# Kernel tuning notes

Hardware: AMD Instinct MI355X
Metric: run time of the kernel (lower is better)

## Reference

```python
import jax, jax.numpy as jnp
import numpy as np
import math

B, T, E, H = 8, 1024, 768, 12
D = E // H  # 64

def setup_inputs() -> dict:
    key = jax.random.key(0)
    ks = jax.random.split(key, 5)
    return {
        "x": jax.random.normal(ks[0], (B, T, E), dtype=jnp.float32),
        "w_attn": jax.random.normal(ks[1], (E, 3 * E), dtype=jnp.float32) * 0.02,
        "b_attn": jax.random.normal(ks[2], (3 * E,), dtype=jnp.float32) * 0.02,
        "w_proj": jax.random.normal(ks[3], (E, E), dtype=jnp.float32) * 0.02,
        "b_proj": jax.random.normal(ks[4], (E,), dtype=jnp.float32) * 0.02,
    }

def reference(x, w_attn, b_attn, w_proj, b_proj):
    b, t, e = x.shape
    h, d = H, E // H
    qkv = x @ w_attn + b_attn                      # [B,T,3E]
    q, k, v = jnp.split(qkv, 3, axis=2)
    q = q.reshape(b, t, h, d).transpose(0, 2, 1, 3)  # [B,H,T,D]
    k = k.reshape(b, t, h, d).transpose(0, 2, 1, 3)
    v = v.reshape(b, t, h, d).transpose(0, 2, 1, 3)
    scores = jnp.einsum('bhqd,bhkd->bhqk', q, k)     # [B,H,T,T]
    causal = jnp.tril(jnp.ones((t, t), dtype=bool))
    scores = jnp.where(causal[None, None], scores, -jnp.inf)
    attn = jax.nn.softmax(scores / jnp.float32(math.sqrt(d)), axis=-1)
    out = jnp.einsum('bhqk,bhkd->bhqd', attn, v)     # [B,H,T,D]
    out = out.transpose(0, 2, 1, 3).reshape(b, t, h * d)
    return out @ w_proj + b_proj
```

## Files before the change

### kernel.cpp

```cpp
#include <hip/hip_runtime.h>
#include <math.h>


#define B_ 8
#define T_ 1024
#define E_ 768
#define H_ 12
#define D_ 64
#define E3 (3 * E_)

typedef __attribute__((ext_vector_type(8))) short bf16x8;
typedef __attribute__((ext_vector_type(4))) float f32x4;

#define SCALE 0.18033688f

__device__ __forceinline__ unsigned short f2bf(float f) {
    unsigned int u = __builtin_bit_cast(unsigned int, f);
    u += 0x7fffu + ((u >> 16) & 1u);
    return (unsigned short)(u >> 16);
}

__device__ __forceinline__ void async_copy16(void* lds, const void* g) {
    __builtin_amdgcn_global_load_lds(
        (const __attribute__((address_space(1))) void*)g,
        (__attribute__((address_space(3))) void*)lds, 16, 0, 0);
}

#define NCVT 6144
#define NTA  (72 * 24)
#define NTP  (24 * 24)

__device__ __forceinline__ void transpose_tile(
    const float* __restrict__ W, unsigned short* __restrict__ Wt,
    int K, int N, int gx, int gy, unsigned short (*tile)[33])
{
    const int n0 = gx * 32, k0 = gy * 32;
    const int tx = threadIdx.x & 31, ty = threadIdx.x >> 5;
    #pragma unroll
    for (int i = 0; i < 4; ++i)
        tile[ty + i * 8][tx] = f2bf(W[(size_t)(k0 + ty + i * 8) * N + n0 + tx]);
    __syncthreads();
    #pragma unroll
    for (int i = 0; i < 4; ++i)
        Wt[(size_t)(n0 + ty + i * 8) * K + k0 + tx] = tile[tx][ty + i * 8];
}

__global__ __launch_bounds__(256) void prep_kernel(
    const float* __restrict__ x, unsigned short* __restrict__ x_bf,
    const float* __restrict__ w_attn, unsigned short* __restrict__ wat,
    const float* __restrict__ w_proj, unsigned short* __restrict__ wpt)
{
    __shared__ unsigned short tile[32][33];
    const int bid = blockIdx.x;
    if (bid < NCVT) {
        const int i = bid * 256 + threadIdx.x;
        float4 f = ((const float4*)x)[i];
        ushort4 o;
        o.x = f2bf(f.x); o.y = f2bf(f.y); o.z = f2bf(f.z); o.w = f2bf(f.w);
        ((ushort4*)x_bf)[i] = o;
    } else if (bid < NCVT + NTA) {
        const int t = bid - NCVT;
        transpose_tile(w_attn, wat, E_, E3, t % 72, t / 72, tile);
    } else {
        const int t = bid - NCVT - NTA;
        transpose_tile(w_proj, wpt, E_, E_, t % 24, t / 24, tile);
    }
}


__global__ __launch_bounds__(512, 4) void gemm_qkv_128x192(
    const unsigned short* __restrict__ A,
    const unsigned short* __restrict__ Wt,
    const float* __restrict__ bias,
    unsigned short* __restrict__ C,
    unsigned short* __restrict__ vt)
{
    constexpr int K = 768;
    constexpr int N = E3;
    constexpr int NKT = 12;

    extern __shared__ unsigned short lds[];

    const int tid  = threadIdx.x;
    const int lane = tid & 63;
    const int w    = tid >> 6;
    const int wm   = w >> 2;
    const int wn   = w & 3;
    const int n16  = lane & 15;
    const int quad = lane >> 4;
    const int l7   = lane & 7;
    const int lrow = lane >> 3;
    const int lcol = (l7 ^ lrow) * 8;

    const int lin  = blockIdx.x;
    const int s    = lin >> 3;
    const int by   = (lin & 7) * 8 + s / 12;
    const int bx   = s % 12;
    const int bm = by * 128, bn = bx * 192;

    const unsigned short* Asrc = A  + (size_t)(bm + lrow) * K + lcol;
    const unsigned short* Bsrc = Wt + (size_t)(bn + lrow) * K + lcol;

    auto stage = [&](int bi, int kt) {
        unsigned short* ab = lds + (bi ? 8192 : 0);
        unsigned short* bb = lds + 16384 + (bi ? 12288 : 0);
        #pragma unroll
        for (int i = 0; i < 2; ++i) {
            const int c = w * 2 + i;
            async_copy16(&ab[c * 512], Asrc + (size_t)(c * 8) * K + kt * 64);
        }
        #pragma unroll
        for (int i = 0; i < 3; ++i) {
            const int c = w * 3 + i;
            async_copy16(&bb[c * 512], Bsrc + (size_t)(c * 8) * K + kt * 64);
        }
    };

    f32x4 acc[4][3] = {};

#define BARR  __builtin_amdgcn_s_barrier()
#define VM5   asm volatile("s_waitcnt vmcnt(5)" ::: "memory")
#define VM0   asm volatile("s_waitcnt vmcnt(0)" ::: "memory")
#define PRI1  __builtin_amdgcn_s_setprio(1)
#define PRI0  __builtin_amdgcn_s_setprio(0)

    stage(0, 0);

    #pragma unroll 1
    for (int u = 0; u < NKT; ++u) {
        const int bi = u & 1;
        const unsigned short* ab = lds + (bi ? 8192 : 0);
        const unsigned short* bb = lds + 16384 + (bi ? 12288 : 0);
        if (u < NKT - 1) {
            stage(bi ^ 1, u + 1);
            VM5;
        } else {
            VM0;
        }
        BARR;

        #pragma unroll
        for (int kc = 0; kc < 2; ++kc) {
            bf16x8 af[4], bf[3];
            #pragma unroll
            for (int m = 0; m < 4; ++m) {
                const int r = wm * 16 + m * 32 + n16;
                af[m] = *(const bf16x8*)&ab[r * 64 + (((kc * 4 + quad) ^ (r & 7)) * 8)];
            }
            #pragma unroll
            for (int n = 0; n < 3; ++n) {
                const int r = wn * 16 + n * 64 + n16;
                bf[n] = *(const bf16x8*)&bb[r * 64 + (((kc * 4 + quad) ^ (r & 7)) * 8)];
            }
            PRI1;
            #pragma unroll
            for (int m = 0; m < 4; ++m)
                #pragma unroll
                for (int n = 0; n < 3; ++n)
                    acc[m][n] = __builtin_amdgcn_mfma_f32_16x16x32_bf16(
                        af[m], bf[n], acc[m][n], 0, 0, 0);
            PRI0;
        }
        BARR;
    }

#undef VM5
#undef VM0

    if (bx >= 8) {
        #pragma unroll
        for (int m = 0; m < 4; ++m) {
            const int tt = bm + wm * 16 + m * 32 + quad * 4;
            const size_t bb2 = (size_t)(tt >> 10) * 768;
            const int tin = tt & 1023;
            #pragma unroll
            for (int n = 0; n < 3; ++n) {
                const int col = bn + wn * 16 + n * 64 + n16;
                const int ch = col - 1536;
                const float bv = bias[col];
                ushort4 o4;
                o4.x = f2bf(acc[m][n][0] + bv);
                o4.y = f2bf(acc[m][n][1] + bv);
                o4.z = f2bf(acc[m][n][2] + bv);
                o4.w = f2bf(acc[m][n][3] + bv);
                *(ushort4*)&vt[(bb2 + ch) * 1024 + tin] = o4;
            }
        }
    } else {
        const bool scale_q = bx < 4;
        #pragma unroll
        for (int m = 0; m < 4; ++m) {
            #pragma unroll
            for (int r = 0; r < 4; ++r) {
                const size_t rowoff = (size_t)(bm + wm * 16 + m * 32 + quad * 4 + r) * N;
                #pragma unroll
                for (int n = 0; n < 3; ++n) {
                    const int col = bn + wn * 16 + n * 64 + n16;
                    float v = acc[m][n][r] + bias[col];
                    if (scale_q) v *= SCALE;
                    C[rowoff + col] = f2bf(v);
                }
            }
        }
    }
}

template <typename OutT, int MODE, int BM, int BN, int WR, int WC>
__global__ __launch_bounds__(256) void gemm_mfma_kernel(
    const unsigned short* __restrict__ A,
    const unsigned short* __restrict__ Wt,
    const float* __restrict__ bias,
    OutT* __restrict__ C,
    unsigned short* __restrict__ vt,
    int M, int N, int K)
{
    constexpr int MT = BM / WR / 16;
    constexpr int NT = BN / WC / 16;
    constexpr int CA = BM / 32;
    constexpr int CB = BN / 32;
    constexpr int QBX = 768 / BN;
    constexpr int VBX = 1536 / BN;

    __shared__ unsigned short Abuf[BM * 64];
    __shared__ unsigned short Bbuf[BN * 64];

    const int tid = threadIdx.x;
    const int lane = tid & 63;
    const int w = tid >> 6;
    const int n16 = lane & 15;
    const int quad = lane >> 4;

    const int nbx = gridDim.x;
    const int lin = blockIdx.y * nbx + blockIdx.x;
    const int band_sz = 8 * nbx;
    const int band = lin / band_sz;
    const int rr = lin % band_sz;
    const int bm = (band * 8 + (rr & 7)) * BM;
    const int bx = rr >> 3;
    const int bn = bx * BN;

    const int wmbase = (w / WC) * (BM / WR);
    const int wnbase = (w % WC) * (BN / WC);

    const int lrow = lane >> 3;
    const int lcol = ((lane & 7) ^ lrow) * 8;

    f32x4 acc[MT][NT] = {};

    for (int k0 = 0; k0 < K; k0 += 64) {
        __syncthreads();
        #pragma unroll
        for (int i = 0; i < CA; ++i) {
            const int c = w * CA + i;
            const int row = c * 8 + lrow;
            async_copy16(&Abuf[c * 512], A + (size_t)(bm + row) * K + k0 + lcol);
        }
        #pragma unroll
        for (int i = 0; i < CB; ++i) {
            const int c = w * CB + i;
            const int row = c * 8 + lrow;
            async_copy16(&Bbuf[c * 512], Wt + (size_t)(bn + row) * K + k0 + lcol);
        }
        __syncthreads();

        #pragma unroll
        for (int kc = 0; kc < 2; ++kc) {
            bf16x8 af[MT], bf[NT];
            #pragma unroll
            for (int mt = 0; mt < MT; ++mt) {
                const int r = wmbase + mt * 16 + n16;
                af[mt] = *(const bf16x8*)&Abuf[r * 64 + ((kc * 4 + quad) ^ (r & 7)) * 8];
            }
            #pragma unroll
            for (int nt = 0; nt < NT; ++nt) {
                const int r = wnbase + nt * 16 + n16;
                bf[nt] = *(const bf16x8*)&Bbuf[r * 64 + ((kc * 4 + quad) ^ (r & 7)) * 8];
            }
            #pragma unroll
            for (int mt = 0; mt < MT; ++mt)
                #pragma unroll
                for (int nt = 0; nt < NT; ++nt)
                    acc[mt][nt] = __builtin_amdgcn_mfma_f32_16x16x32_bf16(
                        af[mt], bf[nt], acc[mt][nt], 0, 0, 0);
        }
    }

    if (MODE == 1 && bx >= VBX) {
        #pragma unroll
        for (int mt = 0; mt < MT; ++mt) {
            const int tt = bm + wmbase + mt * 16 + quad * 4;
            const size_t bb = (size_t)(tt >> 10) * 768;
            const int tin = tt & 1023;
            #pragma unroll
            for (int nt = 0; nt < NT; ++nt) {
                const int col = bn + wnbase + nt * 16 + n16;
                const int ch = col - 1536;
                const float bv = bias[col];
                ushort4 o4;
                o4.x = f2bf(acc[mt][nt][0] + bv);
                o4.y = f2bf(acc[mt][nt][1] + bv);
                o4.z = f2bf(acc[mt][nt][2] + bv);
                o4.w = f2bf(acc[mt][nt][3] + bv);
                *(ushort4*)&vt[(bb + ch) * 1024 + tin] = o4;
            }
        }
        return;
    }

    const bool scale_q = (MODE == 1) && (bx < QBX);
    #pragma unroll
    for (int mt = 0; mt < MT; ++mt) {
        #pragma unroll
        for (int r = 0; r < 4; ++r) {
            const size_t rowoff = (size_t)(bm + wmbase + mt * 16 + quad * 4 + r) * N;
            #pragma unroll
            for (int nt = 0; nt < NT; ++nt) {
                const int col = bn + wnbase + nt * 16 + n16;
                float v = acc[mt][nt][r] + bias[col];
                if (scale_q) v *= SCALE;
                if constexpr (sizeof(OutT) == 2) C[rowoff + col] = (OutT)f2bf(v);
                else                             C[rowoff + col] = (OutT)v;
            }
        }
    }
}

#define BKEY 128

__global__ __launch_bounds__(256, 3) void flash_attn_kernel(
    const unsigned short* __restrict__ qkv,
    const unsigned short* __restrict__ vt,
    unsigned short* __restrict__ out)
{
    __shared__ __align__(16) unsigned short Ks[2][BKEY * 64];
    __shared__ __align__(16) unsigned short Vts[64 * BKEY];

    const int tid = threadIdx.x;
    const int idx = blockIdx.x;
    const int xcd = idx & 7;
    const int j   = idx >> 3;
    const int head = xcd * 12 + (j % 12);
    const int p    = j / 12;
    const int h = head % H_;
    const int b = head / H_;

    const int lane = tid & 63;
    const int w    = tid >> 6;
    const int n16  = lane & 15;
    const int quad = lane >> 4;

    const size_t base = (size_t)b * T_ * E3;
    const unsigned short* qbase = qkv + base + h * D_;
    const unsigned short* kbase = qkv + base + E_ + h * D_;
    const unsigned short* vtb   = vt + (size_t)(b * H_ + h) * 64 * 1024;

    const int lrow = lane >> 3;
    const int lcol = ((lane & 7) ^ lrow) * 8;
    const int vr4 = lane >> 4;
    const int vc  = lane & 15;

    const int qtA = p, qtB = 15 - p;
    const int nIterA = (qtA + 2) >> 1;
    const int nIterB = (qtB + 2) >> 1;
    const int wqA = qtA * 64 + w * 16;
    const int wqB = qtB * 64 + w * 16;

    const unsigned short* qrpA = qbase + (size_t)(wqA + n16) * E3 + quad * 8;
    bf16x8 qfA0 = *(const bf16x8*)qrpA;
    bf16x8 qfA1 = *(const bf16x8*)(qrpA + 32);
    const unsigned short* qrpB = qbase + (size_t)(wqB + n16) * E3 + quad * 8;
    bf16x8 qfB0 = *(const bf16x8*)qrpB;
    bf16x8 qfB1 = *(const bf16x8*)(qrpB + 32);

    f32x4 oA[4] = {}, oB[4] = {};
    float lsA = 0.f, lsB = 0.f;

    const int sLo = n16 + 32 * (quad & 1);
    const int sHi = sLo + 16;
    const bool hiSel = quad >= 2;

    auto stageK = [&](int t) {
        unsigned short* dst = Ks[t & 1];
        const int k0 = t * BKEY;
        #pragma unroll
        for (int i = 0; i < 4; ++i) {
            const int c = w * 4 + i;
            const int row = c * 8 + lrow;
            async_copy16(&dst[c * 512], kbase + (size_t)(k0 + row) * E3 + lcol);
        }
    };
    auto stageV = [&](int t) {
        const int k0 = t * BKEY;
        #pragma unroll
        for (int i = 0; i < 4; ++i) {
            const int jj = w * 4 + i;
            const int row = 4 * jj + vr4;
            async_copy16(&Vts[4 * jj * BKEY],
                         vtb + (size_t)row * 1024 + k0 + ((vc ^ (row & 15)) * 8));
        }
    };

    auto phase = [&](bf16x8 qf0, bf16x8 qf1, f32x4* o, float& lsum,
                     int wave_q_min, int k0, const unsigned short* Kb,
                     bool doMid, bool notLast) {
        int knt_lim = ((wave_q_min + 15 - k0) >> 4) + 1;
        if (knt_lim > 8) knt_lim = 8;
        const int ks_lim = (knt_lim + 1) >> 1;
        const int nkp = ks_lim * 2;
        int Ab2 = wave_q_min - k0 - 15;
        int kfull = Ab2 < 0 ? 0 : (Ab2 >> 4) + 1;
        if (kfull > 8) kfull = 8;

        const int qcol = wave_q_min + n16;

        f32x4 s[8];
        #pragma unroll
        for (int knt = 0; knt < 8; ++knt) {
            if (knt < knt_lim) {
                const int r = knt * 16 + n16;
                bf16x8 kf0 = *(const bf16x8*)&Kb[r * 64 + ((0 + quad) ^ (r & 7)) * 8];
                bf16x8 kf1 = *(const bf16x8*)&Kb[r * 64 + ((4 + quad) ^ (r & 7)) * 8];
                f32x4 acc = {0.f, 0.f, 0.f, 0.f};
                acc = __builtin_amdgcn_mfma_f32_16x16x32_bf16(kf0, qf0, acc, 0, 0, 0);
                acc = __builtin_amdgcn_mfma_f32_16x16x32_bf16(kf1, qf1, acc, 0, 0, 0);
                s[knt] = acc;
            }
        }
        #pragma unroll
        for (int knt = 0; knt < 8; ++knt) {
            if (knt >= kfull && knt < nkp) {
                const int krow = k0 + knt * 16 + quad * 4;
                #pragma unroll
                for (int r = 0; r < 4; ++r) {
                    float v = (knt < knt_lim) ? s[knt][r] : -1e30f;
                    if (krow + r > qcol) v = -1e30f;
                    s[knt][r] = v;
                }
            }
        }

        unsigned int e0[8], e1[8];
        #pragma unroll
        for (int knt = 0; knt < 8; ++knt) {
            if (knt < nkp) {
                float pv0 = __builtin_amdgcn_exp2f(s[knt][0]);
                float pv1 = __builtin_amdgcn_exp2f(s[knt][1]);
                float pv2 = __builtin_amdgcn_exp2f(s[knt][2]);
                float pv3 = __builtin_amdgcn_exp2f(s[knt][3]);
                lsum += (pv0 + pv1) + (pv2 + pv3);
                unsigned int u0 = __builtin_bit_cast(unsigned int, pv0);
                unsigned int u1 = __builtin_bit_cast(unsigned int, pv1);
                unsigned int u2 = __builtin_bit_cast(unsigned int, pv2);
                unsigned int u3 = __builtin_bit_cast(unsigned int, pv3);
                e0[knt] = ((u0 + 0x8000u) >> 16) | ((u1 + 0x8000u) & 0xffff0000u);
                e1[knt] = ((u2 + 0x8000u) >> 16) | ((u3 + 0x8000u) & 0xffff0000u);
            }
        }

        if (doMid) {
            if (notLast) asm volatile("s_waitcnt vmcnt(4)" ::: "memory");
            else         asm volatile("s_waitcnt vmcnt(0)" ::: "memory");
            __builtin_amdgcn_s_barrier();
        }

        #pragma unroll
        for (int ks = 0; ks < 4; ++ks) {
            if (ks < ks_lim) {
                const int kA = 2 * ks, kB = 2 * ks + 1;
                unsigned int a0 = (unsigned)__shfl((int)e0[kA], sLo);
                unsigned int a1 = (unsigned)__shfl((int)e1[kA], sLo);
                unsigned int a2 = (unsigned)__shfl((int)e0[kA], sHi);
                unsigned int a3 = (unsigned)__shfl((int)e1[kA], sHi);
                unsigned int b0 = (unsigned)__shfl((int)e0[kB], sLo);
                unsigned int b1 = (unsigned)__shfl((int)e1[kB], sLo);
                unsigned int b2 = (unsigned)__shfl((int)e0[kB], sHi);
                unsigned int b3 = (unsigned)__shfl((int)e1[kB], sHi);
                uint4 pu;
                pu.x = hiSel ? b0 : a0;
                pu.y = hiSel ? b1 : a1;
                pu.z = hiSel ? b2 : a2;
                pu.w = hiSel ? b3 : a3;
                bf16x8 pf = __builtin_bit_cast(bf16x8, pu);
                #pragma unroll
                for (int dt = 0; dt < 4; ++dt) {
                    const int row = dt * 16 + n16;
                    bf16x8 vf = *(const bf16x8*)&Vts[row * BKEY +
                                    (((ks * 4 + quad) ^ n16) * 8)];
                    o[dt] = __builtin_amdgcn_mfma_f32_16x16x32_bf16(pf, vf, o[dt], 0, 0, 0);
                }
            }
        }
    };

    stageK(0);
    asm volatile("s_waitcnt vmcnt(0)" ::: "memory");
    __builtin_amdgcn_s_barrier();

    for (int it = 0; it < nIterB; ++it) {
        const int k0 = it * BKEY;
        const bool notLast = (it + 1 < nIterB);

        stageV(it);
        if (notLast) stageK(it + 1);
        const unsigned short* Kb = Ks[it & 1];

        phase(qfB0, qfB1, oB, lsB, wqB, k0, Kb, true,  notLast);
        if (it < nIterA)
            phase(qfA0, qfA1, oA, lsA, wqA, k0, Kb, false, notLast);

        asm volatile("s_waitcnt vmcnt(0)" ::: "memory");
        __builtin_amdgcn_s_barrier();
    }

    lsA += __shfl_xor(lsA, 16); lsA += __shfl_xor(lsA, 32);
    lsB += __shfl_xor(lsB, 16); lsB += __shfl_xor(lsB, 32);

    #pragma unroll
    for (int r = 0; r < 4; ++r) {
        const float invA = 1.f / __shfl(lsA, quad * 4 + r);
        unsigned short* orowA = out + ((size_t)b * T_ + wqA + quad * 4 + r) * E_ + h * D_;
        #pragma unroll
        for (int dt = 0; dt < 4; ++dt)
            orowA[dt * 16 + n16] = f2bf(oA[dt][r] * invA);
        const float invB = 1.f / __shfl(lsB, quad * 4 + r);
        unsigned short* orowB = out + ((size_t)b * T_ + wqB + quad * 4 + r) * E_ + h * D_;
        #pragma unroll
        for (int dt = 0; dt < 4; ++dt)
            orowB[dt * 16 + n16] = f2bf(oB[dt][r] * invB);
    }
}

extern "C" void kernel_launch(void* const* d_in, const int* in_sizes, int n_in,
                              void* d_out, int out_size, void* d_ws, size_t ws_size,
                              hipStream_t stream)
{
    const float* x      = (const float*)d_in[0];
    const float* w_attn = (const float*)d_in[1];
    const float* b_attn = (const float*)d_in[2];
    const float* w_proj = (const float*)d_in[3];
    const float* b_proj = (const float*)d_in[4];
    float* out = (float*)d_out;

    const int M = B_ * T_;

    unsigned short* x_bf   = (unsigned short*)d_ws;
    unsigned short* wat    = x_bf + (size_t)M * E_;
    unsigned short* wpt    = wat + (size_t)E3 * E_;
    unsigned short* qkv_bf = wpt + (size_t)E_ * E_;
    unsigned short* att_bf = qkv_bf + (size_t)M * E3;
    unsigned short* vt_bf  = att_bf + (size_t)M * E_;

    static bool qkv_attr_set = false;
    if (!qkv_attr_set) {
        (void)hipFuncSetAttribute((const void*)gemm_qkv_128x192,
                                  hipFuncAttributeMaxDynamicSharedMemorySize, 81920);
        qkv_attr_set = true;
    }

    prep_kernel<<<NCVT + NTA + NTP, 256, 0, stream>>>(x, x_bf, w_attn, wat, w_proj, wpt);

    gemm_qkv_128x192<<<dim3(768), dim3(512), 81920, stream>>>(
        x_bf, wat, b_attn, qkv_bf, vt_bf);

    flash_attn_kernel<<<B_ * H_ * 8, 256, 0, stream>>>(qkv_bf, vt_bf, att_bf);

    gemm_mfma_kernel<float, 0, 64, 128, 2, 2>
        <<<dim3(E_ / 128, M / 64), 256, 0, stream>>>(
        att_bf, wpt, b_proj, out, nullptr, M, E_, E_);
}
```

Baseline: 167.2 us.

## Unify QKV and output projections into one templated double-buffered 128x96 GEMM

Replaces the 512-thread 128x192 QKV GEMM and the single-buffered 64x128 output-projection GEMM with one templated 256-thread kernel using 128x96 tiles and double-buffered async global-to-LDS loads. The output projection gains load/compute overlap it lacked before, and the QKV GEMM now runs more, smaller blocks. The hipFuncSetAttribute call for 81920 bytes of dynamic LDS is removed because the new kernel requests 57344 bytes. Smaller N tiles lower per-block reuse of the A operand and raise the number of barriers per output element.

```diff
diff --git a/kernel.cpp b/kernel.cpp
--- a/kernel.cpp
+++ b/kernel.cpp
@@ -68,58 +68,64 @@
 }
 
 
-__global__ __launch_bounds__(512, 4) void gemm_qkv_128x192(
+template <typename OutT, int MODE, int N_>
+__global__ __launch_bounds__(256, 2) void gemm_2ph(
     const unsigned short* __restrict__ A,
     const unsigned short* __restrict__ Wt,
     const float* __restrict__ bias,
-    unsigned short* __restrict__ C,
+    OutT* __restrict__ C,
     unsigned short* __restrict__ vt)
 {
     constexpr int K = 768;
-    constexpr int N = E3;
     constexpr int NKT = 12;
+    constexpr int NBX = N_ / 96;
+    constexpr int QBX = 768 / 96;
+    constexpr int VBX = 1536 / 96;
 
     extern __shared__ unsigned short lds[];
 
     const int tid  = threadIdx.x;
     const int lane = tid & 63;
     const int w    = tid >> 6;
-    const int wm   = w >> 2;
-    const int wn   = w & 3;
+    const int wm   = w >> 1;
+    const int wn   = w & 1;
     const int n16  = lane & 15;
     const int quad = lane >> 4;
-    const int l7   = lane & 7;
-    const int lrow = lane >> 3;
-    const int lcol = (l7 ^ lrow) * 8;
-
-    const int lin  = blockIdx.x;
-    const int s    = lin >> 3;
-    const int by   = (lin & 7) * 8 + s / 12;
-    const int bx   = s % 12;
-    const int bm = by * 128, bn = bx * 192;
-
-    const unsigned short* Asrc = A  + (size_t)(bm + lrow) * K + lcol;
-    const unsigned short* Bsrc = Wt + (size_t)(bn + lrow) * K + lcol;
+
+    const int lin = blockIdx.x;
+    const int s   = lin >> 3;
+    const int by  = (lin & 7) * 8 + s / NBX;
+    const int bx  = s % NBX;
+    const int bm = by * 128, bn = bx * 96;
+
+    const unsigned short* Asrc = A  + (size_t)bm * K;
+    const unsigned short* Bsrc = Wt + (size_t)bn * K;
 
     auto stage = [&](int bi, int kt) {
         unsigned short* ab = lds + (bi ? 8192 : 0);
-        unsigned short* bb = lds + 16384 + (bi ? 12288 : 0);
-        #pragma unroll
-        for (int i = 0; i < 2; ++i) {
-            const int c = w * 2 + i;
-            async_copy16(&ab[c * 512], Asrc + (size_t)(c * 8) * K + kt * 64);
+        unsigned short* bb = lds + 16384 + (bi ? 6144 : 0);
+        #pragma unroll
+        for (int i = 0; i < 4; ++i) {
+            const int li = i * 256 + tid;
+            const int row = li >> 3;
+            const int sl  = li & 7;
+            async_copy16(&ab[li * 8],
+                         Asrc + (size_t)row * K + ((sl ^ (row & 7)) * 8) + kt * 64);
         }
         #pragma unroll
         for (int i = 0; i < 3; ++i) {
-            const int c = w * 3 + i;
-            async_copy16(&bb[c * 512], Bsrc + (size_t)(c * 8) * K + kt * 64);
+            const int li = i * 256 + tid;
+            const int row = li >> 3;
+            const int sl  = li & 7;
+            async_copy16(&bb[li * 8],
+                         Bsrc + (size_t)row * K + ((sl ^ (row & 7)) * 8) + kt * 64);
         }
     };
 
     f32x4 acc[4][3] = {};
 
 #define BARR  __builtin_amdgcn_s_barrier()
-#define VM5   asm volatile("s_waitcnt vmcnt(5)" ::: "memory")
+#define VM7   asm volatile("s_waitcnt vmcnt(7)" ::: "memory")
 #define VM0   asm volatile("s_waitcnt vmcnt(0)" ::: "memory")
 #define PRI1  __builtin_amdgcn_s_setprio(1)
 #define PRI0  __builtin_amdgcn_s_setprio(0)
@@ -130,10 +136,10 @@
     for (int u = 0; u < NKT; ++u) {
         const int bi = u & 1;
         const unsigned short* ab = lds + (bi ? 8192 : 0);
-        const unsigned short* bb = lds + 16384 + (bi ? 12288 : 0);
+        const unsigned short* bb = lds + 16384 + (bi ? 6144 : 0);
         if (u < NKT - 1) {
             stage(bi ^ 1, u + 1);
-            VM5;
+            VM7;
         } else {
             VM0;
         }
@@ -149,7 +155,7 @@
             }
             #pragma unroll
             for (int n = 0; n < 3; ++n) {
-                const int r = wn * 16 + n * 64 + n16;
+                const int r = wn * 16 + n * 32 + n16;
                 bf[n] = *(const bf16x8*)&bb[r * 64 + (((kc * 4 + quad) ^ (r & 7)) * 8)];
             }
             PRI1;
@@ -164,10 +170,10 @@
         BARR;
     }
 
-#undef VM5
+#undef VM7
 #undef VM0
 
-    if (bx >= 8) {
+    if (MODE == 1 && bx >= VBX) {
         #pragma unroll
         for (int m = 0; m < 4; ++m) {
             const int tt = bm + wm * 16 + m * 32 + quad * 4;
@@ -175,7 +181,7 @@
             const int tin = tt & 1023;
             #pragma unroll
             for (int n = 0; n < 3; ++n) {
-                const int col = bn + wn * 16 + n * 64 + n16;
+                const int col = bn + wn * 16 + n * 32 + n16;
                 const int ch = col - 1536;
                 const float bv = bias[col];
                 ushort4 o4;
@@ -186,137 +192,19 @@
                 *(ushort4*)&vt[(bb2 + ch) * 1024 + tin] = o4;
             }
         }
-    } else {
-        const bool scale_q = bx < 4;
-        #pragma unroll
-        for (int m = 0; m < 4; ++m) {
-            #pragma unroll
-            for (int r = 0; r < 4; ++r) {
-                const size_t rowoff = (size_t)(bm + wm * 16 + m * 32 + quad * 4 + r) * N;
-                #pragma unroll
-                for (int n = 0; n < 3; ++n) {
-                    const int col = bn + wn * 16 + n * 64 + n16;
-                    float v = acc[m][n][r] + bias[col];
-                    if (scale_q) v *= SCALE;
-                    C[rowoff + col] = f2bf(v);
-                }
-            }
-        }
-    }
-}
-
-template <typename OutT, int MODE, int BM, int BN, int WR, int WC>
-__global__ __launch_bounds__(256) void gemm_mfma_kernel(
-    const unsigned short* __restrict__ A,
-    const unsigned short* __restrict__ Wt,
-    const float* __restrict__ bias,
-    OutT* __restrict__ C,
-    unsigned short* __restrict__ vt,
-    int M, int N, int K)
-{
-    constexpr int MT = BM / WR / 16;
-    constexpr int NT = BN / WC / 16;
-    constexpr int CA = BM / 32;
-    constexpr int CB = BN / 32;
-    constexpr int QBX = 768 / BN;
-    constexpr int VBX = 1536 / BN;
-
-    __shared__ unsigned short Abuf[BM * 64];
-    __shared__ unsigned short Bbuf[BN * 64];
-
-    const int tid = threadIdx.x;
-    const int lane = tid & 63;
-    const int w = tid >> 6;
-    const int n16 = lane & 15;
-    const int quad = lane >> 4;
-
-    const int nbx = gridDim.x;
-    const int lin = blockIdx.y * nbx + blockIdx.x;
-    const int band_sz = 8 * nbx;
-    const int band = lin / band_sz;
-    const int rr = lin % band_sz;
-    const int bm = (band * 8 + (rr & 7)) * BM;
-    const int bx = rr >> 3;
-    const int bn = bx * BN;
-
-    const int wmbase = (w / WC) * (BM / WR);
-    const int wnbase = (w % WC) * (BN / WC);
-
-    const int lrow = lane >> 3;
-    const int lcol = ((lane & 7) ^ lrow) * 8;
-
-    f32x4 acc[MT][NT] = {};
-
-    for (int k0 = 0; k0 < K; k0 += 64) {
-        __syncthreads();
-        #pragma unroll
-        for (int i = 0; i < CA; ++i) {
-            const int c = w * CA + i;
-            const int row = c * 8 + lrow;
-            async_copy16(&Abuf[c * 512], A + (size_t)(bm + row) * K + k0 + lcol);
-        }
-        #pragma unroll
-        for (int i = 0; i < CB; ++i) {
-            const int c = w * CB + i;
-            const int row = c * 8 + lrow;
-            async_copy16(&Bbuf[c * 512], Wt + (size_t)(bn + row) * K + k0 + lcol);
-        }
-        __syncthreads();
-
-        #pragma unroll
-        for (int kc = 0; kc < 2; ++kc) {
-            bf16x8 af[MT], bf[NT];
-            #pragma unroll
-            for (int mt = 0; mt < MT; ++mt) {
-                const int r = wmbase + mt * 16 + n16;
-                af[mt] = *(const bf16x8*)&Abuf[r * 64 + ((kc * 4 + quad) ^ (r & 7)) * 8];
-            }
-            #pragma unroll
-            for (int nt = 0; nt < NT; ++nt) {
-                const int r = wnbase + nt * 16 + n16;
-                bf[nt] = *(const bf16x8*)&Bbuf[r * 64 + ((kc * 4 + quad) ^ (r & 7)) * 8];
-            }
-            #pragma unroll
-            for (int mt = 0; mt < MT; ++mt)
-                #pragma unroll
-                for (int nt = 0; nt < NT; ++nt)
-                    acc[mt][nt] = __builtin_amdgcn_mfma_f32_16x16x32_bf16(
-                        af[mt], bf[nt], acc[mt][nt], 0, 0, 0);
-        }
-    }
-
-    if (MODE == 1 && bx >= VBX) {
-        #pragma unroll
-        for (int mt = 0; mt < MT; ++mt) {
-            const int tt = bm + wmbase + mt * 16 + quad * 4;
-            const size_t bb = (size_t)(tt >> 10) * 768;
-            const int tin = tt & 1023;
-            #pragma unroll
-            for (int nt = 0; nt < NT; ++nt) {
-                const int col = bn + wnbase + nt * 16 + n16;
-                const int ch = col - 1536;
-                const float bv = bias[col];
-                ushort4 o4;
-                o4.x = f2bf(acc[mt][nt][0] + bv);
-                o4.y = f2bf(acc[mt][nt][1] + bv);
-                o4.z = f2bf(acc[mt][nt][2] + bv);
-                o4.w = f2bf(acc[mt][nt][3] + bv);
-                *(ushort4*)&vt[(bb + ch) * 1024 + tin] = o4;
-            }
-        }
         return;
     }
 
     const bool scale_q = (MODE == 1) && (bx < QBX);
     #pragma unroll
-    for (int mt = 0; mt < MT; ++mt) {
+    for (int m = 0; m < 4; ++m) {
         #pragma unroll
         for (int r = 0; r < 4; ++r) {
-            const size_t rowoff = (size_t)(bm + wmbase + mt * 16 + quad * 4 + r) * N;
+            const size_t rowoff = (size_t)(bm + wm * 16 + m * 32 + quad * 4 + r) * N_;
             #pragma unroll
-            for (int nt = 0; nt < NT; ++nt) {
-                const int col = bn + wnbase + nt * 16 + n16;
-                float v = acc[mt][nt][r] + bias[col];
+            for (int n = 0; n < 3; ++n) {
+                const int col = bn + wn * 16 + n * 32 + n16;
+                float v = acc[m][n][r] + bias[col];
                 if (scale_q) v *= SCALE;
                 if constexpr (sizeof(OutT) == 2) C[rowoff + col] = (OutT)f2bf(v);
                 else                             C[rowoff + col] = (OutT)v;
@@ -550,21 +438,13 @@
     unsigned short* att_bf = qkv_bf + (size_t)M * E3;
     unsigned short* vt_bf  = att_bf + (size_t)M * E_;
 
-    static bool qkv_attr_set = false;
-    if (!qkv_attr_set) {
-        (void)hipFuncSetAttribute((const void*)gemm_qkv_128x192,
-                                  hipFuncAttributeMaxDynamicSharedMemorySize, 81920);
-        qkv_attr_set = true;
-    }
-
     prep_kernel<<<NCVT + NTA + NTP, 256, 0, stream>>>(x, x_bf, w_attn, wat, w_proj, wpt);
 
-    gemm_qkv_128x192<<<dim3(768), dim3(512), 81920, stream>>>(
+    gemm_2ph<unsigned short, 1, E3><<<dim3(1536), dim3(256), 57344, stream>>>(
         x_bf, wat, b_attn, qkv_bf, vt_bf);
 
     flash_attn_kernel<<<B_ * H_ * 8, 256, 0, stream>>>(qkv_bf, vt_bf, att_bf);
 
-    gemm_mfma_kernel<float, 0, 64, 128, 2, 2>
-        <<<dim3(E_ / 128, M / 64), 256, 0, stream>>>(
-        att_bf, wpt, b_proj, out, nullptr, M, E_, E_);
-}
+    gemm_2ph<float, 0, E_><<<dim3(512), dim3(256), 57344, stream>>>(
+        att_bf, wpt, b_proj, out, nullptr);
+}
```

Measured after the change: 174.2 us. 1.04x slower.

## Enlarge QKV GEMM tile to 256x288 with interleaved staged loads

Applied to the files above, without the earlier changes.

Replaces the 128x192 QKV GEMM tile with a 256x288 tile per 512-thread block, reducing the grid to 256 blocks (one per CU) and raising data reuse per LDS load. The K-loop is split into six sub-phases that interleave LDS fragment reads, partial async global-to-LDS prefetches of the next tile, and MFMA groups, with fine-grained vmcnt waits. The aim is to cut global/LDS traffic per FLOP and overlap loads with compute, at the cost of higher register and LDS use (lower occupancy) and many more barriers.

```diff
diff --git a/kernel.cpp b/kernel.cpp
--- a/kernel.cpp
+++ b/kernel.cpp
@@ -67,8 +67,7 @@
     }
 }
 
-
-__global__ __launch_bounds__(512, 4) void gemm_qkv_128x192(
+__global__ __launch_bounds__(512, 2) void gemm_qkv_288(
     const unsigned short* __restrict__ A,
     const unsigned short* __restrict__ Wt,
     const float* __restrict__ bias,
@@ -76,7 +75,6 @@
     unsigned short* __restrict__ vt)
 {
     constexpr int K = 768;
-    constexpr int N = E3;
     constexpr int NKT = 12;
 
     extern __shared__ unsigned short lds[];
@@ -84,122 +82,148 @@
     const int tid  = threadIdx.x;
     const int lane = tid & 63;
     const int w    = tid >> 6;
-    const int wm   = w >> 2;
-    const int wn   = w & 3;
+    const int wm   = w & 3;
+    const int wn   = w >> 2;
     const int n16  = lane & 15;
     const int quad = lane >> 4;
     const int l7   = lane & 7;
     const int lrow = lane >> 3;
     const int lcol = (l7 ^ lrow) * 8;
 
-    const int lin  = blockIdx.x;
-    const int s    = lin >> 3;
-    const int by   = (lin & 7) * 8 + s / 12;
-    const int bx   = s % 12;
-    const int bm = by * 128, bn = bx * 192;
-
-    const unsigned short* Asrc = A  + (size_t)(bm + lrow) * K + lcol;
-    const unsigned short* Bsrc = Wt + (size_t)(bn + lrow) * K + lcol;
-
-    auto stage = [&](int bi, int kt) {
-        unsigned short* ab = lds + (bi ? 8192 : 0);
-        unsigned short* bb = lds + 16384 + (bi ? 12288 : 0);
-        #pragma unroll
-        for (int i = 0; i < 2; ++i) {
-            const int c = w * 2 + i;
-            async_copy16(&ab[c * 512], Asrc + (size_t)(c * 8) * K + kt * 64);
-        }
-        #pragma unroll
-        for (int i = 0; i < 3; ++i) {
-            const int c = w * 3 + i;
-            async_copy16(&bb[c * 512], Bsrc + (size_t)(c * 8) * K + kt * 64);
-        }
-    };
-
-    f32x4 acc[4][3] = {};
+    const int lin = blockIdx.x;
+    const int j   = lin >> 3;
+    const int by  = (lin & 7) * 4 + (j & 3);
+    const int bx  = j >> 2;
+    const int bm = by * 256, bn = bx * 288;
+
+    const unsigned short* Asrc = A  + (size_t)bm * K;
+    const unsigned short* Bsrc = Wt + (size_t)bn * K;
+
+    auto stA0 = [&](int bi, int kt) {
+        unsigned short* ab = lds + (bi ? 16384 : 0);
+        #pragma unroll
+        for (int s = 0; s < 2; ++s) {
+            const int c = w * 2 + s;
+            async_copy16(&ab[c * 512], Asrc + (size_t)(c * 8 + lrow) * K + kt * 64 + lcol);
+        }
+    };
+    auto stA1 = [&](int bi, int kt) {
+        unsigned short* ab = lds + (bi ? 16384 : 0);
+        #pragma unroll
+        for (int s = 0; s < 2; ++s) {
+            const int c = 16 + w * 2 + s;
+            async_copy16(&ab[c * 512], Asrc + (size_t)(c * 8 + lrow) * K + kt * 64 + lcol);
+        }
+    };
+    auto stB01 = [&](int g, int bi, int kt) {
+        unsigned short* bb = lds + 32768 + (bi ? 18432 : 0);
+        #pragma unroll
+        for (int s = 0; s < 2; ++s) {
+            const int c = g * 16 + w * 2 + s;
+            async_copy16(&bb[c * 512], Bsrc + (size_t)(c * 8 + lrow) * K + kt * 64 + lcol);
+        }
+    };
+    auto stB2 = [&](int bi, int kt) {
+        unsigned short* bb = lds + 32768 + (bi ? 18432 : 0);
+        const int c = (w < 4) ? (32 + w) : (w - 4);
+        async_copy16(&bb[c * 512], Bsrc + (size_t)(c * 8 + lrow) * K + kt * 64 + lcol);
+    };
+
+    bf16x8 a0f[4], a1f[4], bfr[6];
+    f32x4 acc[4][9] = {};
 
 #define BARR  __builtin_amdgcn_s_barrier()
+#define LGKM0 asm volatile("s_waitcnt lgkmcnt(0)" ::: "memory")
+#define VM3   asm volatile("s_waitcnt vmcnt(3)" ::: "memory")
 #define VM5   asm volatile("s_waitcnt vmcnt(5)" ::: "memory")
-#define VM0   asm volatile("s_waitcnt vmcnt(0)" ::: "memory")
+#define VM8   asm volatile("s_waitcnt vmcnt(8)" ::: "memory")
 #define PRI1  __builtin_amdgcn_s_setprio(1)
 #define PRI0  __builtin_amdgcn_s_setprio(0)
 
-    stage(0, 0);
+#define LDA_(dst, QM) { \
+    _Pragma("unroll") \
+    for (int ml = 0; ml < 2; ++ml) { \
+        const int r = wm * 16 + ((QM) * 2 + ml) * 64 + n16; \
+        const unsigned short* rp = ab + r * 64; \
+        dst[ml * 2 + 0] = *(const bf16x8*)&rp[((0 + quad) ^ (r & 7)) * 8]; \
+        dst[ml * 2 + 1] = *(const bf16x8*)&rp[((4 + quad) ^ (r & 7)) * 8]; \
+    } }
+#define LDB_(QT) { \
+    _Pragma("unroll") \
+    for (int nl = 0; nl < 3; ++nl) { \
+        const int r = wn * 16 + ((QT) * 3 + nl) * 32 + n16; \
+        const unsigned short* rp = bb + r * 64; \
+        bfr[nl * 2 + 0] = *(const bf16x8*)&rp[((0 + quad) ^ (r & 7)) * 8]; \
+        bfr[nl * 2 + 1] = *(const bf16x8*)&rp[((4 + quad) ^ (r & 7)) * 8]; \
+    } }
+#define MM_(QM, QT, AF) { \
+    _Pragma("unroll") \
+    for (int ml = 0; ml < 2; ++ml) \
+    _Pragma("unroll") \
+    for (int nl = 0; nl < 3; ++nl) \
+    _Pragma("unroll") \
+    for (int kk = 0; kk < 2; ++kk) \
+        acc[(QM) * 2 + ml][(QT) * 3 + nl] = __builtin_amdgcn_mfma_f32_16x16x32_bf16( \
+            AF[ml * 2 + kk], bfr[nl * 2 + kk], acc[(QM) * 2 + ml][(QT) * 3 + nl], 0, 0, 0); }
+
+    stA0(0, 0); stA1(0, 0); stB01(0, 0, 0); stB01(1, 0, 0); stB2(0, 0);
+    asm volatile("s_waitcnt vmcnt(0)" ::: "memory");
+    BARR;
 
     #pragma unroll 1
-    for (int u = 0; u < NKT; ++u) {
-        const int bi = u & 1;
-        const unsigned short* ab = lds + (bi ? 8192 : 0);
-        const unsigned short* bb = lds + 16384 + (bi ? 12288 : 0);
-        if (u < NKT - 1) {
-            stage(bi ^ 1, u + 1);
-            VM5;
-        } else {
-            VM0;
-        }
-        BARR;
-
-        #pragma unroll
-        for (int kc = 0; kc < 2; ++kc) {
-            bf16x8 af[4], bf[3];
-            #pragma unroll
-            for (int m = 0; m < 4; ++m) {
-                const int r = wm * 16 + m * 32 + n16;
-                af[m] = *(const bf16x8*)&ab[r * 64 + (((kc * 4 + quad) ^ (r & 7)) * 8)];
-            }
-            #pragma unroll
-            for (int n = 0; n < 3; ++n) {
-                const int r = wn * 16 + n * 64 + n16;
-                bf[n] = *(const bf16x8*)&bb[r * 64 + (((kc * 4 + quad) ^ (r & 7)) * 8)];
-            }
-            PRI1;
-            #pragma unroll
-            for (int m = 0; m < 4; ++m)
+    for (int t = 0; t < NKT; ++t) {
+        const int bi = t & 1;
+        const unsigned short* ab = lds + (bi ? 16384 : 0);
+        const unsigned short* bb = lds + 32768 + (bi ? 18432 : 0);
+        const bool st = (t < NKT - 1);
+
+        LDA_(a0f, 0); LDB_(0);
+        if (st) stA0(bi ^ 1, t + 1);
+        BARR; LGKM0; PRI1; MM_(0, 0, a0f); PRI0; BARR;
+        LDA_(a1f, 1);
+        if (st) stA1(bi ^ 1, t + 1);
+        BARR; LGKM0; PRI1; MM_(1, 0, a1f); PRI0; VM5; BARR;
+        LDB_(1);
+        if (st) stB01(0, bi ^ 1, t + 1);
+        BARR; LGKM0; PRI1; MM_(1, 1, a1f); PRI0; BARR;
+        if (st) stB01(1, bi ^ 1, t + 1);
+        BARR; LGKM0; PRI1; MM_(0, 1, a0f); PRI0; VM8; BARR;
+        LDB_(2);
+        if (st) stB2(bi ^ 1, t + 1);
+        BARR; LGKM0; PRI1; MM_(0, 2, a0f); PRI0; BARR;
+        BARR; LGKM0; PRI1; MM_(1, 2, a1f); PRI0; VM3; BARR;
+    }
+
+#undef LDA_
+#undef LDB_
+#undef MM_
+#undef VM3
+#undef VM5
+#undef VM8
+
+    #pragma unroll
+    for (int mt = 0; mt < 4; ++mt) {
+        const int rowb = bm + wm * 16 + mt * 64 + quad * 4;
+        #pragma unroll
+        for (int nt = 0; nt < 9; ++nt) {
+            const int cb = bn + wn * 16 + nt * 32;
+            const int col = cb + n16;
+            const float bv = bias[col];
+            if (cb < 1536) {
+                const float sc = (cb < 768) ? SCALE : 1.0f;
                 #pragma unroll
-                for (int n = 0; n < 3; ++n)
-                    acc[m][n] = __builtin_amdgcn_mfma_f32_16x16x32_bf16(
-                        af[m], bf[n], acc[m][n], 0, 0, 0);
-            PRI0;
-        }
-        BARR;
-    }
-
-#undef VM5
-#undef VM0
-
-    if (bx >= 8) {
-        #pragma unroll
-        for (int m = 0; m < 4; ++m) {
-            const int tt = bm + wm * 16 + m * 32 + quad * 4;
-            const size_t bb2 = (size_t)(tt >> 10) * 768;
-            const int tin = tt & 1023;
-            #pragma unroll
-            for (int n = 0; n < 3; ++n) {
-                const int col = bn + wn * 16 + n * 64 + n16;
+                for (int r = 0; r < 4; ++r)
+                    C[(size_t)(rowb + r) * E3 + col] = f2bf((acc[mt][nt][r] + bv) * sc);
+            } else {
+                const size_t bb2 = (size_t)(rowb >> 10) * 768;
+                const int tin = rowb & 1023;
                 const int ch = col - 1536;
-                const float bv = bias[col];
                 ushort4 o4;
-                o4.x = f2bf(acc[m][n][0] + bv);
-                o4.y = f2bf(acc[m][n][1] + bv);
-                o4.z = f2bf(acc[m][n][2] + bv);
-                o4.w = f2bf(acc[m][n][3] + bv);
+                o4.x = f2bf(acc[mt][nt][0] + bv);
+                o4.y = f2bf(acc[mt][nt][1] + bv);
+                o4.z = f2bf(acc[mt][nt][2] + bv);
+                o4.w = f2bf(acc[mt][nt][3] + bv);
                 *(ushort4*)&vt[(bb2 + ch) * 1024 + tin] = o4;
-            }
-        }
-    } else {
-        const bool scale_q = bx < 4;
-        #pragma unroll
-        for (int m = 0; m < 4; ++m) {
-            #pragma unroll
-            for (int r = 0; r < 4; ++r) {
-                const size_t rowoff = (size_t)(bm + wm * 16 + m * 32 + quad * 4 + r) * N;
-                #pragma unroll
-                for (int n = 0; n < 3; ++n) {
-                    const int col = bn + wn * 16 + n * 64 + n16;
-                    float v = acc[m][n][r] + bias[col];
-                    if (scale_q) v *= SCALE;
-                    C[rowoff + col] = f2bf(v);
-                }
             }
         }
     }
@@ -552,14 +576,14 @@
 
     static bool qkv_attr_set = false;
     if (!qkv_attr_set) {
-        (void)hipFuncSetAttribute((const void*)gemm_qkv_128x192,
-                                  hipFuncAttributeMaxDynamicSharedMemorySize, 81920);
+        (void)hipFuncSetAttribute((const void*)gemm_qkv_288,
+                                  hipFuncAttributeMaxDynamicSharedMemorySize, 139264);
         qkv_attr_set = true;
     }
 
     prep_kernel<<<NCVT + NTA + NTP, 256, 0, stream>>>(x, x_bf, w_attn, wat, w_proj, wpt);
 
-    gemm_qkv_128x192<<<dim3(768), dim3(512), 81920, stream>>>(
+    gemm_qkv_288<<<dim3(256), dim3(512), 139264, stream>>>(
         x_bf, wat, b_attn, qkv_bf, vt_bf);
 
     flash_attn_kernel<<<B_ * H_ * 8, 256, 0, stream>>>(qkv_bf, vt_bf, att_bf);
```

Measured after the change: 172.8 us. +3.3%, slower.
